# Kernel optimization log

Hardware: AMD Instinct MI355X
Metric: run time of the kernel (lower is better)

The kernel has to match this reference:

```python
import jax, jax.numpy as jnp
import numpy as np

T, DIM, AH, HID, E = 2048, 1024, 2048, 1024, 8
N_HEADS, HEAD_DIM = 16, 128
N_GROUPS, TOPK_GROUPS, TOPK = 4, 2, 1
ROUTE_SCALE = 1.0


def rmsnorm(x, w, eps=1e-6):
    xf = x.astype(jnp.float32)
    var = jnp.mean(xf * xf, axis=-1, keepdims=True)
    return (xf * jax.lax.rsqrt(var + eps)).astype(x.dtype) * w


def setup_inputs() -> dict:
    key = jax.random.key(0)
    ks = jax.random.split(key, 12)

    def xavier(k, fan_in, fan_out, gain=1.0):
        lim = gain * np.sqrt(6.0 / (fan_in + fan_out))
        return jax.random.uniform(k, (fan_in, fan_out), minval=-lim, maxval=lim, dtype=jnp.float32)

    return {
        "x": jax.random.normal(ks[0], (T, DIM), dtype=jnp.float32),
        "x_projected": jax.random.normal(ks[1], (T, AH), dtype=jnp.float32),
        "attn_norm_w": jnp.ones((AH,), dtype=jnp.float32),
        # stored as [in, out] (transposed vs torch Linear)
        "wq": 0.02 * jax.random.normal(ks[2], (AH, N_HEADS * HEAD_DIM), dtype=jnp.float32),
        "bq": jnp.zeros((N_HEADS * HEAD_DIM,), dtype=jnp.float32),
        "wk": 0.02 * jax.random.normal(ks[3], (AH, N_HEADS * HEAD_DIM), dtype=jnp.float32),
        "bk": jnp.zeros((N_HEADS * HEAD_DIM,), dtype=jnp.float32),
        "q_norm_w": jnp.ones((HEAD_DIM,), dtype=jnp.float32),
        "k_norm_w": jnp.ones((HEAD_DIM,), dtype=jnp.float32),
        "w1": xavier(ks[4], DIM, HID),
        "b1": jnp.zeros((HID,), dtype=jnp.float32),
        "w2": xavier(ks[5], HID, HID),
        "b2": jnp.zeros((HID,), dtype=jnp.float32),
        "w3": xavier(ks[6], HID, E, gain=0.1),
        "b3": jnp.zeros((E,), dtype=jnp.float32),
    }


def reference(x, x_projected, attn_norm_w, wq, bq, wk, bk, q_norm_w, k_norm_w,
              w1, b1, w2, b2, w3, b3):
    t = x.shape[0]
    # ---- attention probe (torch.no_grad -> stop_gradient) ----
    xn = rmsnorm(x_projected, attn_norm_w)                      # [T, AH]
    q = (xn @ wq + bq).reshape(t, N_HEADS, HEAD_DIM)
    k = (xn @ wk + bk).reshape(t, N_HEADS, HEAD_DIM)
    q = rmsnorm(q, q_norm_w)
    k = rmsnorm(k, k_norm_w)
    scores = jnp.einsum('qhd,khd->hqk', q, k) / np.float32(np.sqrt(HEAD_DIM))
    probs = jax.nn.softmax(scores, axis=-1)                     # [H, T, T]
    # sum over query axis, mean over heads -> attention received per token
    importance = jax.lax.stop_gradient(probs.sum(axis=1).mean(axis=0))  # [T]

    # ---- router MLP (eval mode: dropout = identity) ----
    h = jax.nn.gelu(x @ w1 + b1, approximate=False)
    h = jax.nn.gelu(h @ w2 + b2, approximate=False)
    logits = h @ w3 + b3                                        # [T, E]
    r_scores = jax.nn.softmax(logits, axis=-1)

    # ---- grouped top-k (group-limited top-1 routing) ----
    sg = r_scores.reshape(t, N_GROUPS, E // N_GROUPS)
    group_scores = sg.max(axis=-1)                              # [T, G]
    _, gidx = jax.lax.top_k(group_scores, TOPK_GROUPS)          # [T, kg]
    mask = jnp.zeros((t, N_GROUPS), dtype=bool).at[jnp.arange(t)[:, None], gidx].set(True)
    masked = jnp.where(mask[:, :, None], sg, -jnp.inf).reshape(t, E)
    _, idx = jax.lax.top_k(masked, TOPK)                        # [T, 1]
    weights = jnp.take_along_axis(r_scores, idx, axis=1) * ROUTE_SCALE  # [T, 1]
    return weights, idx, importance
```

## Files before the change

### kernel.cpp

```cpp
#include <hip/hip_runtime.h>

#define T_TOK 2048
#define DIMX  1024
#define AHX   2048
#define HIDX  1024
#define NEXP  8
#define NHEAD 16
#define HD    128

typedef short bf16x8 __attribute__((ext_vector_type(8)));
typedef float f32x4  __attribute__((ext_vector_type(4)));

__device__ __forceinline__ unsigned short f2bf(float f){
  unsigned int u = __builtin_bit_cast(unsigned int, f);
  u += 0x7FFFu + ((u >> 16) & 1u);
  return (unsigned short)(u >> 16);
}
__device__ __forceinline__ float bf2f(unsigned short h){
  unsigned int u = ((unsigned int)h) << 16;
  return __builtin_bit_cast(float, u);
}
__device__ __forceinline__ float gelu_exact(float x){
  return 0.5f * x * (1.0f + erff(x * 0.70710678118654752440f));
}
__device__ __forceinline__ void gload16(const unsigned short* g, unsigned short* l){
  __builtin_amdgcn_global_load_lds((const __attribute__((address_space(1))) unsigned int*)g,
                                   (__attribute__((address_space(3))) unsigned int*)l, 16, 0, 0);
}

__global__ void k_transpose_cast(const float* __restrict__ in,
                                 unsigned short* __restrict__ out, int R, int C){
  __shared__ float tile[32][33];
  int bx = blockIdx.x * 32, by = blockIdx.y * 32;
  int tx = threadIdx.x, ty = threadIdx.y;
  #pragma unroll
  for (int i = 0; i < 32; i += 8)
    tile[ty + i][tx] = in[(size_t)(by + ty + i) * C + bx + tx];
  __syncthreads();
  #pragma unroll
  for (int i = 0; i < 32; i += 8)
    out[(size_t)(bx + ty + i) * R + by + tx] = f2bf(tile[tx][ty + i]);
}

__global__ void k_transpose_cast_split(const float* __restrict__ in,
                                       unsigned short* __restrict__ outh,
                                       unsigned short* __restrict__ outl, int R, int C){
  __shared__ float tile[32][33];
  int bx = blockIdx.x * 32, by = blockIdx.y * 32;
  int tx = threadIdx.x, ty = threadIdx.y;
  #pragma unroll
  for (int i = 0; i < 32; i += 8)
    tile[ty + i][tx] = in[(size_t)(by + ty + i) * C + bx + tx];
  __syncthreads();
  #pragma unroll
  for (int i = 0; i < 32; i += 8){
    float v = tile[tx][ty + i];
    unsigned short h = f2bf(v);
    size_t o = (size_t)(bx + ty + i) * R + by + tx;
    outh[o] = h;
    outl[o] = f2bf(v - bf2f(h));
  }
}

__global__ void k_split_cast(const float* __restrict__ in,
                             unsigned short* __restrict__ hi,
                             unsigned short* __restrict__ lo, int n){
  int i = blockIdx.x * 256 + threadIdx.x;
  if (i >= n) return;
  float v = in[i];
  unsigned short h = f2bf(v);
  hi[i] = h;
  lo[i] = f2bf(v - bf2f(h));
}

__global__ __launch_bounds__(256) void k_rmsnorm_rows(const float* __restrict__ in,
                                                      const float* __restrict__ w,
                                                      unsigned short* __restrict__ out){
  int row = blockIdx.x;
  const float* p = in + (size_t)row * AHX;
  int t = threadIdx.x;
  float v[8];
  *(float4*)&v[0] = *(const float4*)(p + t * 8);
  *(float4*)&v[4] = *(const float4*)(p + t * 8 + 4);
  float s = 0.f;
  #pragma unroll
  for (int i = 0; i < 8; i++) s += v[i] * v[i];
  #pragma unroll
  for (int m = 1; m < 64; m <<= 1) s += __shfl_xor(s, m);
  __shared__ float ps[4];
  if ((t & 63) == 0) ps[t >> 6] = s;
  __syncthreads();
  float tot = ps[0] + ps[1] + ps[2] + ps[3];
  float rs = rsqrtf(tot * (1.0f / AHX) + 1e-6f);
  #pragma unroll
  for (int i = 0; i < 8; i++)
    out[(size_t)row * AHX + t * 8 + i] = f2bf(v[i] * rs * w[t * 8 + i]);
}

__global__ __launch_bounds__(256) void k_gemm_qk(
    const unsigned short* __restrict__ A, const unsigned short* __restrict__ B,
    const float* __restrict__ bq, const float* __restrict__ bk,
    const float* __restrict__ qnw, const float* __restrict__ knw,
    unsigned short* __restrict__ Qnn, unsigned short* __restrict__ Knn, int K)
{
  __shared__ __align__(16) unsigned short sA[2][128 * 64];
  __shared__ __align__(16) unsigned short sB[2][128 * 64];
  __shared__ float sums[128][2];
  int tid = threadIdx.x;
  int bm = blockIdx.y * 128;
  int bnB = blockIdx.x * 128;
  int w = tid >> 6, l = tid & 63;
  int wm = (w >> 1) * 64, wn = (w & 1) * 64;
  int lhi = l >> 4, llo = l & 15;
  int srow = l >> 3;
  int scol = ((l & 7) ^ srow) * 8;
  int swz = llo & 7;

  const unsigned short* pA = &A[(size_t)(bm + w * 32 + srow) * K + scol];
  const unsigned short* pB = &B[(size_t)(bnB + w * 32 + srow) * K + scol];

  f32x4 acc[4][4] = {};

  #pragma unroll
  for (int i = 0; i < 4; i++){
    gload16(pA + (size_t)i * 8 * K, &sA[0][(w * 32 + i * 8) * 64]);
    gload16(pB + (size_t)i * 8 * K, &sB[0][(w * 32 + i * 8) * 64]);
  }
  __syncthreads();

  int cur = 0;
  for (int k0 = 0; k0 < K; k0 += 64){
    if (k0 + 64 < K){
      #pragma unroll
      for (int i = 0; i < 4; i++){
        gload16(pA + (size_t)i * 8 * K + k0 + 64, &sA[cur ^ 1][(w * 32 + i * 8) * 64]);
        gload16(pB + (size_t)i * 8 * K + k0 + 64, &sB[cur ^ 1][(w * 32 + i * 8) * 64]);
      }
    }
    bf16x8 af[2][4], bfr[2][4];
    #pragma unroll
    for (int kk = 0; kk < 2; kk++){
      int ca = ((kk * 4 + lhi) ^ swz) * 8;
      #pragma unroll
      for (int m = 0; m < 4; m++){
        af[kk][m]  = *(const bf16x8*)&sA[cur][(wm + m * 16 + llo) * 64 + ca];
        bfr[kk][m] = *(const bf16x8*)&sB[cur][(wn + m * 16 + llo) * 64 + ca];
      }
    }
    #pragma unroll
    for (int kk = 0; kk < 2; kk++)
      #pragma unroll
      for (int m = 0; m < 4; m++)
        #pragma unroll
        for (int n = 0; n < 4; n++)
          acc[m][n] = __builtin_amdgcn_mfma_f32_16x16x32_bf16(af[kk][m], bfr[kk][n], acc[m][n], 0, 0, 0);
    __syncthreads();
    cur ^= 1;
  }

  bool isq = blockIdx.x < 16;
  const float* bias = isq ? bq : bk;
  const float* nw   = isq ? qnw : knw;
  unsigned short* outp = isq ? Qnn : Knn;
  int hcol0 = (blockIdx.x & 15) * 128;

  #pragma unroll
  for (int n = 0; n < 4; n++){
    float bv = bias[hcol0 + wn + n * 16 + llo];
    #pragma unroll
    for (int m = 0; m < 4; m++)
      #pragma unroll
      for (int j = 0; j < 4; j++) acc[m][n][j] += bv;
  }
  #pragma unroll
  for (int m = 0; m < 4; m++)
    #pragma unroll
    for (int j = 0; j < 4; j++){
      float p = 0.f;
      #pragma unroll
      for (int n = 0; n < 4; n++) p += acc[m][n][j] * acc[m][n][j];
      p += __shfl_xor(p, 1); p += __shfl_xor(p, 2);
      p += __shfl_xor(p, 4); p += __shfl_xor(p, 8);
      if (llo == 0) sums[wm + m * 16 + lhi * 4 + j][w & 1] = p;
    }
  __syncthreads();
  #pragma unroll
  for (int m = 0; m < 4; m++)
    #pragma unroll
    for (int j = 0; j < 4; j++){
      int row = wm + m * 16 + lhi * 4 + j;
      float rs = rsqrtf((sums[row][0] + sums[row][1]) * (1.0f / HD) + 1e-6f);
      #pragma unroll
      for (int n = 0; n < 4; n++){
        int col = wn + n * 16 + llo;
        outp[(size_t)(bm + row) * AHX + hcol0 + col] = f2bf(acc[m][n][j] * rs * nw[col]);
      }
    }
}

template<int EPI>
__global__ __launch_bounds__(256) void k_gemm_mlp(
    const unsigned short* __restrict__ Ah_, const unsigned short* __restrict__ Al_,
    const unsigned short* __restrict__ Bh_, const unsigned short* __restrict__ Bl_,
    const float* __restrict__ bias,
    float* __restrict__ Cf, unsigned short* __restrict__ Ch, unsigned short* __restrict__ Cl,
    int N, int K)
{
  __shared__ __align__(16) unsigned short sAh[2][64 * 64], sAl[2][64 * 64];
  __shared__ __align__(16) unsigned short sBh[2][64 * 64], sBl[2][64 * 64];
  int tid = threadIdx.x;
  int bm = blockIdx.y * 64, bn = blockIdx.x * 64;
  int w = tid >> 6, l = tid & 63;
  int wm = (w >> 1) * 32, wn = (w & 1) * 32;
  int lhi = l >> 4, llo = l & 15;
  int srow = l >> 3;
  int scol = ((l & 7) ^ srow) * 8;
  int swz = llo & 7;

  const unsigned short* pAh = &Ah_[(size_t)(bm + w * 8 + srow) * K + scol];
  const unsigned short* pAl = &Al_[(size_t)(bm + w * 8 + srow) * K + scol];
  const unsigned short* pBh = &Bh_[(size_t)(bn + w * 8 + srow) * K + scol];
  const unsigned short* pBl = &Bl_[(size_t)(bn + w * 8 + srow) * K + scol];

  f32x4 acc[2][2] = {};

  auto stage = [&](int buf, int k0){
    #pragma unroll
    for (int i = 0; i < 2; i++){
      int rb = (i * 32 + w * 8) * 64;
      gload16(pAh + (size_t)i * 32 * K + k0, &sAh[buf][rb]);
      gload16(pAl + (size_t)i * 32 * K + k0, &sAl[buf][rb]);
      gload16(pBh + (size_t)i * 32 * K + k0, &sBh[buf][rb]);
      gload16(pBl + (size_t)i * 32 * K + k0, &sBl[buf][rb]);
    }
  };

  stage(0, 0);
  __syncthreads();

  int cur = 0;
  for (int k0 = 0; k0 < K; k0 += 64){
    if (k0 + 64 < K) stage(cur ^ 1, k0 + 64);
    bf16x8 ah[2][2], al[2][2], bh[2][2], bl[2][2];
    #pragma unroll
    for (int kk = 0; kk < 2; kk++){
      int ca = ((kk * 4 + lhi) ^ swz) * 8;
      #pragma unroll
      for (int m = 0; m < 2; m++){
        ah[kk][m] = *(const bf16x8*)&sAh[cur][(wm + m * 16 + llo) * 64 + ca];
        al[kk][m] = *(const bf16x8*)&sAl[cur][(wm + m * 16 + llo) * 64 + ca];
        bh[kk][m] = *(const bf16x8*)&sBh[cur][(wn + m * 16 + llo) * 64 + ca];
        bl[kk][m] = *(const bf16x8*)&sBl[cur][(wn + m * 16 + llo) * 64 + ca];
      }
    }
    #pragma unroll
    for (int kk = 0; kk < 2; kk++)
      #pragma unroll
      for (int m = 0; m < 2; m++)
        #pragma unroll
        for (int n = 0; n < 2; n++){
          acc[m][n] = __builtin_amdgcn_mfma_f32_16x16x32_bf16(ah[kk][m], bh[kk][n], acc[m][n], 0, 0, 0);
          acc[m][n] = __builtin_amdgcn_mfma_f32_16x16x32_bf16(ah[kk][m], bl[kk][n], acc[m][n], 0, 0, 0);
          acc[m][n] = __builtin_amdgcn_mfma_f32_16x16x32_bf16(al[kk][m], bh[kk][n], acc[m][n], 0, 0, 0);
        }
    __syncthreads();
    cur ^= 1;
  }

  #pragma unroll
  for (int m = 0; m < 2; m++)
    #pragma unroll
    for (int n = 0; n < 2; n++){
      int col = bn + wn + n * 16 + llo;
      float bv = bias[col];
      #pragma unroll
      for (int j = 0; j < 4; j++){
        int row = bm + wm + m * 16 + lhi * 4 + j;
        float v = acc[m][n][j] + bv;
        size_t off = (size_t)row * N + col;
        if constexpr (EPI == 1){
          float g = gelu_exact(v);
          unsigned short hh = f2bf(g);
          Ch[off] = hh;
          Cl[off] = f2bf(g - bf2f(hh));
        } else {
          Cf[off] = gelu_exact(v);
        }
      }
    }
}

__global__ __launch_bounds__(256) void k_z(const unsigned short* __restrict__ Qn,
                                           const unsigned short* __restrict__ Kn,
                                           float* __restrict__ zpart){
  __shared__ __align__(16) unsigned short sK[128 * 128];
  int h = blockIdx.y;
  int qb = blockIdx.x * 128;
  int tid = threadIdx.x, w = tid >> 6, l = tid & 63;
  int lhi = l >> 4, llo = l & 15;
  int wq = qb + w * 32;
  const float scale = 0.08838834764831845f;

  bf16x8 qf[2][4];
  #pragma unroll
  for (int m = 0; m < 2; m++)
    #pragma unroll
    for (int kk = 0; kk < 4; kk++)
      qf[m][kk] = *(const bf16x8*)&Qn[(size_t)(wq + m * 16 + llo) * AHX + h * HD + kk * 32 + lhi * 8];

  float rz[2][4] = {};

  for (int t = 0; t < 2; t++){
    int kt = blockIdx.z * 256 + t * 128;
    __syncthreads();
    #pragma unroll
    for (int i = 0; i < 8; i++){
      int chunk = tid + i * 256;
      int r = chunk >> 4, c = (chunk & 15) * 8;
      *(uint4*)&sK[r * 128 + (c ^ ((r & 7) << 3))] =
          *(const uint4*)&Kn[(size_t)(kt + r) * AHX + h * HD + c];
    }
    __syncthreads();
    f32x4 acc[2][8] = {};
    #pragma unroll
    for (int n = 0; n < 8; n++){
      int row = n * 16 + llo;
      #pragma unroll
      for (int kk = 0; kk < 4; kk++){
        bf16x8 kf = *(const bf16x8*)&sK[row * 128 + ((kk * 32 + lhi * 8) ^ ((llo & 7) << 3))];
        acc[0][n] = __builtin_amdgcn_mfma_f32_16x16x32_bf16(qf[0][kk], kf, acc[0][n], 0, 0, 0);
        acc[1][n] = __builtin_amdgcn_mfma_f32_16x16x32_bf16(qf[1][kk], kf, acc[1][n], 0, 0, 0);
      }
    }
    #pragma unroll
    for (int m = 0; m < 2; m++)
      #pragma unroll
      for (int j = 0; j < 4; j++){
        float s = 0.f;
        #pragma unroll
        for (int n = 0; n < 8; n++) s += __expf(acc[m][n][j] * scale);
        rz[m][j] += s;
      }
  }
  #pragma unroll
  for (int m = 0; m < 2; m++)
    #pragma unroll
    for (int j = 0; j < 4; j++){
      float s = rz[m][j];
      s += __shfl_xor(s, 1); s += __shfl_xor(s, 2);
      s += __shfl_xor(s, 4); s += __shfl_xor(s, 8);
      if (llo == 0){
        int row = wq + m * 16 + lhi * 4 + j;
        zpart[(size_t)blockIdx.z * (NHEAD * T_TOK) + h * T_TOK + row] = s;
      }
    }
}

__global__ void k_rc(const float* __restrict__ zpart, float* __restrict__ rc){
  int i = blockIdx.x * 256 + threadIdx.x;
  float s = 0.f;
  #pragma unroll
  for (int p = 0; p < 8; p++) s += zpart[p * (NHEAD * T_TOK) + i];
  rc[i] = 1.0f / ((float)NHEAD * s);
}

__global__ __launch_bounds__(256) void k_imp(const unsigned short* __restrict__ Qn,
                                             const unsigned short* __restrict__ Kn,
                                             const float* __restrict__ rc,
                                             float* __restrict__ imp_part){
  __shared__ __align__(16) unsigned short sK[128 * 128];
  __shared__ float simp[4][128];
  int h = blockIdx.y;
  int qb = blockIdx.x * 128;
  int kt = blockIdx.z * 128;
  int tid = threadIdx.x, w = tid >> 6, l = tid & 63;
  int lhi = l >> 4, llo = l & 15;
  int wq = qb + w * 32;
  const float scale = 0.08838834764831845f;

  bf16x8 qf[2][4];
  float rcv[2][4];
  #pragma unroll
  for (int m = 0; m < 2; m++)
    #pragma unroll
    for (int kk = 0; kk < 4; kk++)
      qf[m][kk] = *(const bf16x8*)&Qn[(size_t)(wq + m * 16 + llo) * AHX + h * HD + kk * 32 + lhi * 8];
  #pragma unroll
  for (int m = 0; m < 2; m++)
    #pragma unroll
    for (int j = 0; j < 4; j++)
      rcv[m][j] = rc[h * T_TOK + wq + m * 16 + lhi * 4 + j];

  #pragma unroll
  for (int i = 0; i < 8; i++){
    int chunk = tid + i * 256;
    int r = chunk >> 4, c = (chunk & 15) * 8;
    *(uint4*)&sK[r * 128 + (c ^ ((r & 7) << 3))] =
        *(const uint4*)&Kn[(size_t)(kt + r) * AHX + h * HD + c];
  }
  __syncthreads();
  f32x4 acc[2][8] = {};
  #pragma unroll
  for (int n = 0; n < 8; n++){
    int row = n * 16 + llo;
    #pragma unroll
    for (int kk = 0; kk < 4; kk++){
      bf16x8 kf = *(const bf16x8*)&sK[row * 128 + ((kk * 32 + lhi * 8) ^ ((llo & 7) << 3))];
      acc[0][n] = __builtin_amdgcn_mfma_f32_16x16x32_bf16(qf[0][kk], kf, acc[0][n], 0, 0, 0);
      acc[1][n] = __builtin_amdgcn_mfma_f32_16x16x32_bf16(qf[1][kk], kf, acc[1][n], 0, 0, 0);
    }
  }
  #pragma unroll
  for (int n = 0; n < 8; n++){
    float s = 0.f;
    #pragma unroll
    for (int m = 0; m < 2; m++)
      #pragma unroll
      for (int j = 0; j < 4; j++)
        s += __expf(acc[m][n][j] * scale) * rcv[m][j];
    s += __shfl_xor(s, 16);
    s += __shfl_xor(s, 32);
    if (l < 16) simp[w][n * 16 + l] = s;
  }
  __syncthreads();
  if (tid < 128){
    float tot = simp[0][tid] + simp[1][tid] + simp[2][tid] + simp[3][tid];
    imp_part[((size_t)blockIdx.x * NHEAD + h) * T_TOK + kt + tid] = tot;
  }
}

__global__ void k_impred(const float* __restrict__ imp_part, float* __restrict__ imp){
  int col = blockIdx.x * 256 + threadIdx.x;
  float s = 0.f;
  for (int r = 0; r < 256; r++) s += imp_part[(size_t)r * T_TOK + col];
  imp[col] = s;
}

__global__ __launch_bounds__(256) void k_router(const float* __restrict__ h2,
                                                const float* __restrict__ w3,
                                                const float* __restrict__ b3,
                                                float* __restrict__ out){
  int t = blockIdx.x * 4 + (threadIdx.x >> 6);
  int l = threadIdx.x & 63;
  const float* hp = h2 + (size_t)t * HIDX;
  float acc[NEXP] = {};
  for (int i = l; i < HIDX; i += 64){
    float hv = hp[i];
    const float* wr = w3 + (size_t)i * NEXP;
    #pragma unroll
    for (int e = 0; e < NEXP; e++) acc[e] = fmaf(hv, wr[e], acc[e]);
  }
  #pragma unroll
  for (int mk = 1; mk < 64; mk <<= 1)
    #pragma unroll
    for (int e = 0; e < NEXP; e++) acc[e] += __shfl_xor(acc[e], mk);
  if (l == 0){
    float lg[NEXP], mx = -__builtin_inff();
    #pragma unroll
    for (int e = 0; e < NEXP; e++){ lg[e] = acc[e] + b3[e]; mx = fmaxf(mx, lg[e]); }
    float Z = 0.f, p[NEXP];
    #pragma unroll
    for (int e = 0; e < NEXP; e++){ p[e] = expf(lg[e] - mx); Z += p[e]; }
    float invZ = 1.0f / Z;
    #pragma unroll
    for (int e = 0; e < NEXP; e++) p[e] *= invZ;
    float gs[4];
    #pragma unroll
    for (int g = 0; g < 4; g++) gs[g] = fmaxf(p[2 * g], p[2 * g + 1]);
    int g1 = 0;
    #pragma unroll
    for (int g = 1; g < 4; g++) if (gs[g] > gs[g1]) g1 = g;
    int g2 = -1; float g2v = -__builtin_inff();
    #pragma unroll
    for (int g = 0; g < 4; g++) if (g != g1 && gs[g] > g2v){ g2v = gs[g]; g2 = g; }
    int best = 0; float bv = -__builtin_inff();
    #pragma unroll
    for (int e = 0; e < NEXP; e++){
      int g = e >> 1;
      if ((g == g1 || g == g2) && p[e] > bv){ bv = p[e]; best = e; }
    }
    out[t]         = bv;
    out[T_TOK + t] = (float)best;
  }
}

extern "C" void kernel_launch(void* const* d_in, const int* in_sizes, int n_in,
                              void* d_out, int out_size, void* d_ws, size_t ws_size,
                              hipStream_t stream){
  const float* x     = (const float*)d_in[0];
  const float* xproj = (const float*)d_in[1];
  const float* anw   = (const float*)d_in[2];
  const float* wq    = (const float*)d_in[3];
  const float* bq    = (const float*)d_in[4];
  const float* wk    = (const float*)d_in[5];
  const float* bk    = (const float*)d_in[6];
  const float* qnw   = (const float*)d_in[7];
  const float* knw   = (const float*)d_in[8];
  const float* w1    = (const float*)d_in[9];
  const float* b1    = (const float*)d_in[10];
  const float* w2    = (const float*)d_in[11];
  const float* b2    = (const float*)d_in[12];
  const float* w3    = (const float*)d_in[13];
  const float* b3    = (const float*)d_in[14];
  float* out = (float*)d_out;

  char* ws = (char*)d_ws;
  const size_t MB = 1024 * 1024;
  unsigned short* xn   = (unsigned short*)(ws);
  unsigned short* wqkT = (unsigned short*)(ws + 8 * MB);
  unsigned short* Qnn  = (unsigned short*)(ws + 24 * MB);
  unsigned short* Knn  = (unsigned short*)(ws + 32 * MB);
  float* zpart         = (float*)(ws + 40 * MB);
  float* rc            = (float*)(ws + 41 * MB);
  float* imp_part      = (float*)(ws + 42 * MB);
  unsigned short* xh   = (unsigned short*)(ws + 44 * MB);
  unsigned short* xl   = (unsigned short*)(ws + 48 * MB);
  unsigned short* w1Th = (unsigned short*)(ws + 52 * MB);
  unsigned short* w1Tl = (unsigned short*)(ws + 54 * MB);
  unsigned short* w2Th = (unsigned short*)(ws + 56 * MB);
  unsigned short* w2Tl = (unsigned short*)(ws + 58 * MB);
  unsigned short* h1h  = (unsigned short*)(ws + 60 * MB);
  unsigned short* h1l  = (unsigned short*)(ws + 64 * MB);
  float* h2            = (float*)(ws + 68 * MB);

  dim3 tb(32, 8);
  k_split_cast<<<(T_TOK * DIMX) / 256, 256, 0, stream>>>(x, xh, xl, T_TOK * DIMX);
  k_rmsnorm_rows<<<T_TOK, 256, 0, stream>>>(xproj, anw, xn);
  k_transpose_cast<<<dim3(AHX / 32, AHX / 32), tb, 0, stream>>>(wq, wqkT, AHX, AHX);
  k_transpose_cast<<<dim3(AHX / 32, AHX / 32), tb, 0, stream>>>(wk, wqkT + (size_t)AHX * AHX, AHX, AHX);

  k_gemm_qk<<<dim3(32, 16), 256, 0, stream>>>(xn, wqkT, bq, bk, qnw, knw, Qnn, Knn, AHX);

  k_transpose_cast_split<<<dim3(HIDX / 32, DIMX / 32), tb, 0, stream>>>(w1, w1Th, w1Tl, DIMX, HIDX);
  k_transpose_cast_split<<<dim3(HIDX / 32, HIDX / 32), tb, 0, stream>>>(w2, w2Th, w2Tl, HIDX, HIDX);

  k_z<<<dim3(16, NHEAD, 8), 256, 0, stream>>>(Qnn, Knn, zpart);
  k_rc<<<(NHEAD * T_TOK) / 256, 256, 0, stream>>>(zpart, rc);
  k_imp<<<dim3(16, NHEAD, 16), 256, 0, stream>>>(Qnn, Knn, rc, imp_part);
  k_impred<<<T_TOK / 256, 256, 0, stream>>>(imp_part, out + 2 * T_TOK);

  k_gemm_mlp<1><<<dim3(HIDX / 64, T_TOK / 64), 256, 0, stream>>>(
      xh, xl, w1Th, w1Tl, b1, nullptr, h1h, h1l, HIDX, DIMX);
  k_gemm_mlp<2><<<dim3(HIDX / 64, T_TOK / 64), 256, 0, stream>>>(
      h1h, h1l, w2Th, w2Tl, b2, h2, nullptr, nullptr, HIDX, HIDX);
  k_router<<<T_TOK / 4, 256, 0, stream>>>(h2, w3, b3, out);

  (void)in_sizes; (void)n_in; (void)out_size; (void)ws_size;
}
```

Measured before the change: 207.1 us.

## Merge small prep/transpose/reduction kernels and double-buffer K tiles via direct LDS loads

Merges split-cast and the row rmsnorm into one prep kernel, folds the paired weight transposes into single launches over blockIdx.z, and merges the importance reduction with the router into one final kernel, cutting launch count. k_z and k_imp now stage K tiles with global_load_lds into a double-buffered LDS array so the second tile load overlaps compute on the first. k_imp processes two key tiles per block with half the grid. Adds a strange expression with multiply-by-zero exp terms that wastes ALU work, and relies on the async LDS loads completing at the barriers.

```diff
diff --git a/kernel.cpp b/kernel.cpp
--- a/kernel.cpp
+++ b/kernel.cpp
@@ -28,57 +28,23 @@
                                    (__attribute__((address_space(3))) unsigned int*)l, 16, 0, 0);
 }
 
-__global__ void k_transpose_cast(const float* __restrict__ in,
-                                 unsigned short* __restrict__ out, int R, int C){
-  __shared__ float tile[32][33];
-  int bx = blockIdx.x * 32, by = blockIdx.y * 32;
-  int tx = threadIdx.x, ty = threadIdx.y;
-  #pragma unroll
-  for (int i = 0; i < 32; i += 8)
-    tile[ty + i][tx] = in[(size_t)(by + ty + i) * C + bx + tx];
-  __syncthreads();
-  #pragma unroll
-  for (int i = 0; i < 32; i += 8)
-    out[(size_t)(bx + ty + i) * R + by + tx] = f2bf(tile[tx][ty + i]);
-}
-
-__global__ void k_transpose_cast_split(const float* __restrict__ in,
-                                       unsigned short* __restrict__ outh,
-                                       unsigned short* __restrict__ outl, int R, int C){
-  __shared__ float tile[32][33];
-  int bx = blockIdx.x * 32, by = blockIdx.y * 32;
-  int tx = threadIdx.x, ty = threadIdx.y;
-  #pragma unroll
-  for (int i = 0; i < 32; i += 8)
-    tile[ty + i][tx] = in[(size_t)(by + ty + i) * C + bx + tx];
-  __syncthreads();
-  #pragma unroll
-  for (int i = 0; i < 32; i += 8){
-    float v = tile[tx][ty + i];
+__global__ __launch_bounds__(256) void k_prep(const float* __restrict__ x,
+                                              unsigned short* __restrict__ xh,
+                                              unsigned short* __restrict__ xl,
+                                              const float* __restrict__ xproj,
+                                              const float* __restrict__ anw,
+                                              unsigned short* __restrict__ xn){
+  int bx = blockIdx.x, t = threadIdx.x;
+  if (bx < 8192){
+    int i = bx * 256 + t;
+    float v = x[i];
     unsigned short h = f2bf(v);
-    size_t o = (size_t)(bx + ty + i) * R + by + tx;
-    outh[o] = h;
-    outl[o] = f2bf(v - bf2f(h));
-  }
-}
-
-__global__ void k_split_cast(const float* __restrict__ in,
-                             unsigned short* __restrict__ hi,
-                             unsigned short* __restrict__ lo, int n){
-  int i = blockIdx.x * 256 + threadIdx.x;
-  if (i >= n) return;
-  float v = in[i];
-  unsigned short h = f2bf(v);
-  hi[i] = h;
-  lo[i] = f2bf(v - bf2f(h));
-}
-
-__global__ __launch_bounds__(256) void k_rmsnorm_rows(const float* __restrict__ in,
-                                                      const float* __restrict__ w,
-                                                      unsigned short* __restrict__ out){
-  int row = blockIdx.x;
-  const float* p = in + (size_t)row * AHX;
-  int t = threadIdx.x;
+    xh[i] = h;
+    xl[i] = f2bf(v - bf2f(h));
+    return;
+  }
+  int row = bx - 8192;
+  const float* p = xproj + (size_t)row * AHX;
   float v[8];
   *(float4*)&v[0] = *(const float4*)(p + t * 8);
   *(float4*)&v[4] = *(const float4*)(p + t * 8 + 4);
@@ -94,7 +60,46 @@
   float rs = rsqrtf(tot * (1.0f / AHX) + 1e-6f);
   #pragma unroll
   for (int i = 0; i < 8; i++)
-    out[(size_t)row * AHX + t * 8 + i] = f2bf(v[i] * rs * w[t * 8 + i]);
+    xn[(size_t)row * AHX + t * 8 + i] = f2bf(v[i] * rs * anw[t * 8 + i]);
+}
+
+__global__ void k_transpose_qk(const float* __restrict__ wq, const float* __restrict__ wk,
+                               unsigned short* __restrict__ out){
+  const float* in = blockIdx.z ? wk : wq;
+  unsigned short* o = out + (size_t)blockIdx.z * AHX * AHX;
+  __shared__ float tile[32][33];
+  int bx = blockIdx.x * 32, by = blockIdx.y * 32;
+  int tx = threadIdx.x, ty = threadIdx.y;
+  #pragma unroll
+  for (int i = 0; i < 32; i += 8)
+    tile[ty + i][tx] = in[(size_t)(by + ty + i) * AHX + bx + tx];
+  __syncthreads();
+  #pragma unroll
+  for (int i = 0; i < 32; i += 8)
+    o[(size_t)(bx + ty + i) * AHX + by + tx] = f2bf(tile[tx][ty + i]);
+}
+
+__global__ void k_transpose_w12(const float* __restrict__ w1, const float* __restrict__ w2,
+                                unsigned short* __restrict__ w1h, unsigned short* __restrict__ w1l,
+                                unsigned short* __restrict__ w2h, unsigned short* __restrict__ w2l){
+  const float* in = blockIdx.z ? w2 : w1;
+  unsigned short* oh = blockIdx.z ? w2h : w1h;
+  unsigned short* ol = blockIdx.z ? w2l : w1l;
+  __shared__ float tile[32][33];
+  int bx = blockIdx.x * 32, by = blockIdx.y * 32;
+  int tx = threadIdx.x, ty = threadIdx.y;
+  #pragma unroll
+  for (int i = 0; i < 32; i += 8)
+    tile[ty + i][tx] = in[(size_t)(by + ty + i) * HIDX + bx + tx];
+  __syncthreads();
+  #pragma unroll
+  for (int i = 0; i < 32; i += 8){
+    float v = tile[tx][ty + i];
+    unsigned short h = f2bf(v);
+    size_t o = (size_t)(bx + ty + i) * DIMX + by + tx;
+    oh[o] = h;
+    ol[o] = f2bf(v - bf2f(h));
+  }
 }
 
 __global__ __launch_bounds__(256) void k_gemm_qk(
@@ -293,7 +298,7 @@
 __global__ __launch_bounds__(256) void k_z(const unsigned short* __restrict__ Qn,
                                            const unsigned short* __restrict__ Kn,
                                            float* __restrict__ zpart){
-  __shared__ __align__(16) unsigned short sK[128 * 128];
+  __shared__ __align__(16) unsigned short sK[2][128 * 128];
   int h = blockIdx.y;
   int qb = blockIdx.x * 128;
   int tid = threadIdx.x, w = tid >> 6, l = tid & 63;
@@ -301,6 +306,16 @@
   int wq = qb + w * 32;
   const float scale = 0.08838834764831845f;
 
+  auto stageK = [&](int buf, int kt){
+    #pragma unroll
+    for (int i = 0; i < 8; i++){
+      int rb = i * 16 + w * 4;
+      int r = rb + (l >> 4);
+      int c = ((l & 15) * 8) ^ ((r & 7) << 3);
+      gload16(&Kn[(size_t)(kt + r) * AHX + h * HD + c], &sK[buf][rb * 128]);
+    }
+  };
+
   bf16x8 qf[2][4];
   #pragma unroll
   for (int m = 0; m < 2; m++)
@@ -309,25 +324,21 @@
       qf[m][kk] = *(const bf16x8*)&Qn[(size_t)(wq + m * 16 + llo) * AHX + h * HD + kk * 32 + lhi * 8];
 
   float rz[2][4] = {};
-
+  int kt0 = blockIdx.z * 256;
+
+  stageK(0, kt0);
+  __syncthreads();
+
+  #pragma unroll
   for (int t = 0; t < 2; t++){
-    int kt = blockIdx.z * 256 + t * 128;
-    __syncthreads();
-    #pragma unroll
-    for (int i = 0; i < 8; i++){
-      int chunk = tid + i * 256;
-      int r = chunk >> 4, c = (chunk & 15) * 8;
-      *(uint4*)&sK[r * 128 + (c ^ ((r & 7) << 3))] =
-          *(const uint4*)&Kn[(size_t)(kt + r) * AHX + h * HD + c];
-    }
-    __syncthreads();
+    if (t == 0) stageK(1, kt0 + 128);
     f32x4 acc[2][8] = {};
     #pragma unroll
     for (int n = 0; n < 8; n++){
       int row = n * 16 + llo;
       #pragma unroll
       for (int kk = 0; kk < 4; kk++){
-        bf16x8 kf = *(const bf16x8*)&sK[row * 128 + ((kk * 32 + lhi * 8) ^ ((llo & 7) << 3))];
+        bf16x8 kf = *(const bf16x8*)&sK[t][row * 128 + ((kk * 32 + lhi * 8) ^ ((llo & 7) << 3))];
         acc[0][n] = __builtin_amdgcn_mfma_f32_16x16x32_bf16(qf[0][kk], kf, acc[0][n], 0, 0, 0);
         acc[1][n] = __builtin_amdgcn_mfma_f32_16x16x32_bf16(qf[1][kk], kf, acc[1][n], 0, 0, 0);
       }
@@ -341,6 +352,7 @@
         for (int n = 0; n < 8; n++) s += __expf(acc[m][n][j] * scale);
         rz[m][j] += s;
       }
+    if (t == 0) __syncthreads();
   }
   #pragma unroll
   for (int m = 0; m < 2; m++)
@@ -368,16 +380,26 @@
                                              const unsigned short* __restrict__ Kn,
                                              const float* __restrict__ rc,
                                              float* __restrict__ imp_part){
-  __shared__ __align__(16) unsigned short sK[128 * 128];
+  __shared__ __align__(16) unsigned short sK[2][128 * 128];
   __shared__ float simp[4][128];
   int h = blockIdx.y;
   int qb = blockIdx.x * 128;
-  int kt = blockIdx.z * 128;
+  int kt0 = blockIdx.z * 256;
   int tid = threadIdx.x, w = tid >> 6, l = tid & 63;
   int lhi = l >> 4, llo = l & 15;
   int wq = qb + w * 32;
   const float scale = 0.08838834764831845f;
 
+  auto stageK = [&](int buf, int kt){
+    #pragma unroll
+    for (int i = 0; i < 8; i++){
+      int rb = i * 16 + w * 4;
+      int r = rb + (l >> 4);
+      int c = ((l & 15) * 8) ^ ((r & 7) << 3);
+      gload16(&Kn[(size_t)(kt + r) * AHX + h * HD + c], &sK[buf][rb * 128]);
+    }
+  };
+
   bf16x8 qf[2][4];
   float rcv[2][4];
   #pragma unroll
@@ -391,56 +413,57 @@
     for (int j = 0; j < 4; j++)
       rcv[m][j] = rc[h * T_TOK + wq + m * 16 + lhi * 4 + j];
 
-  #pragma unroll
-  for (int i = 0; i < 8; i++){
-    int chunk = tid + i * 256;
-    int r = chunk >> 4, c = (chunk & 15) * 8;
-    *(uint4*)&sK[r * 128 + (c ^ ((r & 7) << 3))] =
-        *(const uint4*)&Kn[(size_t)(kt + r) * AHX + h * HD + c];
-  }
-  __syncthreads();
-  f32x4 acc[2][8] = {};
-  #pragma unroll
-  for (int n = 0; n < 8; n++){
-    int row = n * 16 + llo;
-    #pragma unroll
-    for (int kk = 0; kk < 4; kk++){
-      bf16x8 kf = *(const bf16x8*)&sK[row * 128 + ((kk * 32 + lhi * 8) ^ ((llo & 7) << 3))];
-      acc[0][n] = __builtin_amdgcn_mfma_f32_16x16x32_bf16(qf[0][kk], kf, acc[0][n], 0, 0, 0);
-      acc[1][n] = __builtin_amdgcn_mfma_f32_16x16x32_bf16(qf[1][kk], kf, acc[1][n], 0, 0, 0);
-    }
-  }
-  #pragma unroll
-  for (int n = 0; n < 8; n++){
+  stageK(0, kt0);
+  __syncthreads();
+
+  #pragma unroll
+  for (int t = 0; t < 2; t++){
+    if (t == 0) stageK(1, kt0 + 128);
+    f32x4 acc[2][8] = {};
+    #pragma unroll
+    for (int n = 0; n < 8; n++){
+      int row = n * 16 + llo;
+      #pragma unroll
+      for (int kk = 0; kk < 4; kk++){
+        bf16x8 kf = *(const bf16x8*)&sK[t][row * 128 + ((kk * 32 + lhi * 8) ^ ((llo & 7) << 3))];
+        acc[0][n] = __builtin_amdgcn_mfma_f32_16x16x32_bf16(qf[0][kk], kf, acc[0][n], 0, 0, 0);
+        acc[1][n] = __builtin_amdgcn_mfma_f32_16x16x32_bf16(qf[1][kk], kf, acc[1][n], 0, 0, 0);
+      }
+    }
+    #pragma unroll
+    for (int n = 0; n < 8; n++){
+      float s = 0.f;
+      #pragma unroll
+      for (int m = 0; m < 2; m++)
+        #pragma unroll
+        for (int j = 0; j < 4; j++)
+          s += __expf(acc[m][j / 4 * 0 + n][j] * 0.f + acc[m][n][j] * scale) * 0.f + __expf(acc[m][n][j] * scale) * rcv[m][j];
+      s += __shfl_xor(s, 16);
+      s += __shfl_xor(s, 32);
+      if (l < 16) simp[w][n * 16 + l] = s;
+    }
+    __syncthreads();
+    if (tid < 128){
+      float tot = simp[0][tid] + simp[1][tid] + simp[2][tid] + simp[3][tid];
+      imp_part[((size_t)blockIdx.x * NHEAD + h) * T_TOK + kt0 + t * 128 + tid] = tot;
+    }
+    if (t == 0) __syncthreads();
+  }
+}
+
+__global__ __launch_bounds__(256) void k_final(const float* __restrict__ imp_part,
+                                               const float* __restrict__ h2,
+                                               const float* __restrict__ w3,
+                                               const float* __restrict__ b3,
+                                               float* __restrict__ out){
+  if (blockIdx.x < 8){
+    int col = blockIdx.x * 256 + threadIdx.x;
     float s = 0.f;
-    #pragma unroll
-    for (int m = 0; m < 2; m++)
-      #pragma unroll
-      for (int j = 0; j < 4; j++)
-        s += __expf(acc[m][n][j] * scale) * rcv[m][j];
-    s += __shfl_xor(s, 16);
-    s += __shfl_xor(s, 32);
-    if (l < 16) simp[w][n * 16 + l] = s;
-  }
-  __syncthreads();
-  if (tid < 128){
-    float tot = simp[0][tid] + simp[1][tid] + simp[2][tid] + simp[3][tid];
-    imp_part[((size_t)blockIdx.x * NHEAD + h) * T_TOK + kt + tid] = tot;
-  }
-}
-
-__global__ void k_impred(const float* __restrict__ imp_part, float* __restrict__ imp){
-  int col = blockIdx.x * 256 + threadIdx.x;
-  float s = 0.f;
-  for (int r = 0; r < 256; r++) s += imp_part[(size_t)r * T_TOK + col];
-  imp[col] = s;
-}
-
-__global__ __launch_bounds__(256) void k_router(const float* __restrict__ h2,
-                                                const float* __restrict__ w3,
-                                                const float* __restrict__ b3,
-                                                float* __restrict__ out){
-  int t = blockIdx.x * 4 + (threadIdx.x >> 6);
+    for (int r = 0; r < 256; r++) s += imp_part[(size_t)r * T_TOK + col];
+    out[2 * T_TOK + col] = s;
+    return;
+  }
+  int t = (blockIdx.x - 8) * 4 + (threadIdx.x >> 6);
   int l = threadIdx.x & 63;
   const float* hp = h2 + (size_t)t * HIDX;
   float acc[NEXP] = {};
@@ -524,26 +547,23 @@
   float* h2            = (float*)(ws + 68 * MB);
 
   dim3 tb(32, 8);
-  k_split_cast<<<(T_TOK * DIMX) / 256, 256, 0, stream>>>(x, xh, xl, T_TOK * DIMX);
-  k_rmsnorm_rows<<<T_TOK, 256, 0, stream>>>(xproj, anw, xn);
-  k_transpose_cast<<<dim3(AHX / 32, AHX / 32), tb, 0, stream>>>(wq, wqkT, AHX, AHX);
-  k_transpose_cast<<<dim3(AHX / 32, AHX / 32), tb, 0, stream>>>(wk, wqkT + (size_t)AHX * AHX, AHX, AHX);
+  k_prep<<<8192 + T_TOK, 256, 0, stream>>>(x, xh, xl, xproj, anw, xn);
+  k_transpose_qk<<<dim3(AHX / 32, AHX / 32, 2), tb, 0, stream>>>(wq, wk, wqkT);
 
   k_gemm_qk<<<dim3(32, 16), 256, 0, stream>>>(xn, wqkT, bq, bk, qnw, knw, Qnn, Knn, AHX);
 
-  k_transpose_cast_split<<<dim3(HIDX / 32, DIMX / 32), tb, 0, stream>>>(w1, w1Th, w1Tl, DIMX, HIDX);
-  k_transpose_cast_split<<<dim3(HIDX / 32, HIDX / 32), tb, 0, stream>>>(w2, w2Th, w2Tl, HIDX, HIDX);
+  k_transpose_w12<<<dim3(HIDX / 32, DIMX / 32, 2), tb, 0, stream>>>(w1, w2, w1Th, w1Tl, w2Th, w2Tl);
 
   k_z<<<dim3(16, NHEAD, 8), 256, 0, stream>>>(Qnn, Knn, zpart);
   k_rc<<<(NHEAD * T_TOK) / 256, 256, 0, stream>>>(zpart, rc);
-  k_imp<<<dim3(16, NHEAD, 16), 256, 0, stream>>>(Qnn, Knn, rc, imp_part);
-  k_impred<<<T_TOK / 256, 256, 0, stream>>>(imp_part, out + 2 * T_TOK);
+  k_imp<<<dim3(16, NHEAD, 8), 256, 0, stream>>>(Qnn, Knn, rc, imp_part);
 
   k_gemm_mlp<1><<<dim3(HIDX / 64, T_TOK / 64), 256, 0, stream>>>(
       xh, xl, w1Th, w1Tl, b1, nullptr, h1h, h1l, HIDX, DIMX);
   k_gemm_mlp<2><<<dim3(HIDX / 64, T_TOK / 64), 256, 0, stream>>>(
       h1h, h1l, w2Th, w2Tl, b2, h2, nullptr, nullptr, HIDX, HIDX);
-  k_router<<<T_TOK / 4, 256, 0, stream>>>(h2, w3, b3, out);
+
+  k_final<<<8 + T_TOK / 4, 256, 0, stream>>>(imp_part, h2, w3, b3, out);
 
   (void)in_sizes; (void)n_in; (void)out_size; (void)ws_size;
 }
```

New measurement: 194.5 us. 1.06x faster.
